# Optimization experiments

Hardware: AMD Instinct MI355X
Metric: run time of the kernel (lower is better)

The kernel has to match this reference:

```python
import jax, jax.numpy as jnp
import numpy as np

# FP4 E2M1 value table (codes 0..7 positive, 8..15 negative, sign in MSB)
FP4_VALUES = jnp.array([0.0, 0.5, 1.0, 1.5, 2.0, 3.0, 4.0, 6.0,
                        -0.0, -0.5, -1.0, -1.5, -2.0, -3.0, -4.0, -6.0],
                       dtype=jnp.float32)


def setup_inputs() -> dict:
    key = jax.random.key(0)
    k1, k2, k3, k4 = jax.random.split(key, 4)
    O, I = 4096, 4096
    block = 16
    x = jax.random.normal(k1, (8192, I), dtype=jnp.float32)
    # packed uint4 pairs stored as int32 bytes in [0, 256)
    weight = jax.random.randint(k2, (O, I // 2), 0, 256, dtype=jnp.int32)
    # per-block FP8-style scales (positive)
    weight_scale = jax.random.uniform(k3, (O, I // block), dtype=jnp.float32, minval=0.01, maxval=1.0)
    bias = jax.random.normal(k4, (O,), dtype=jnp.float32)
    return {"x": x, "weight": weight, "weight_scale": weight_scale,
            "bias": bias, "block_size": block}


def _dequant_nvfp4(weight, weight_scale, block_size):
    # unpack two FP4 codes per byte: high nibble is the even (first) element
    hi = (weight >> 4) & 0xF
    lo = weight & 0xF
    O = weight.shape[0]
    codes = jnp.stack([hi, lo], axis=-1).reshape(O, -1)  # [O, I]
    vals = FP4_VALUES[codes]                             # [O, I] f32
    I = vals.shape[1]
    # apply per-block scale
    w = vals.reshape(O, I // block_size, block_size) * weight_scale[:, :, None]
    return w.reshape(O, I)


def reference(x, weight, weight_scale, bias, block_size):
    w = _dequant_nvfp4(weight, weight_scale, block_size)  # [O, I]
    return jnp.einsum('ti,oi->to', x, w) + bias[None, :]
```

## Files before the change

### kernel.cpp

```cpp
#include <hip/hip_runtime.h>
#include <hip/hip_fp16.h>

typedef __attribute__((ext_vector_type(8))) _Float16 f16x8;
typedef __attribute__((ext_vector_type(4))) float f32x4;

#define M_DIM 8192
#define N_DIM 4096
#define K_DIM 4096
#define BM 256
#define BN 256
#define BK 64
#define NT (K_DIM / BK)
#define ITERS (NT / 2)

__constant__ float FP4_LUT[16] = {0.f, 0.5f, 1.f, 1.5f, 2.f, 3.f, 4.f, 6.f,
                                  -0.f, -0.5f, -1.f, -1.5f, -2.f, -3.f, -4.f, -6.f};

__device__ inline void glds16(const void* g, void* l) {
    __builtin_amdgcn_global_load_lds(
        (const __attribute__((address_space(1))) void*)g,
        (__attribute__((address_space(3))) void*)l, 16, 0, 0);
}

__global__ __launch_bounds__(256) void cvt_x_kernel(const float* __restrict__ x,
                                                    _Float16* __restrict__ xh) {
    int i = (blockIdx.x * 256 + threadIdx.x) * 8;
    const float4* p = (const float4*)(x + i);
    float4 a = p[0], b = p[1];
    f16x8 h;
    h[0] = (_Float16)a.x; h[1] = (_Float16)a.y;
    h[2] = (_Float16)a.z; h[3] = (_Float16)a.w;
    h[4] = (_Float16)b.x; h[5] = (_Float16)b.y;
    h[6] = (_Float16)b.z; h[7] = (_Float16)b.w;
    *(f16x8*)(xh + i) = h;
}

__global__ __launch_bounds__(256) void dequant_w_kernel(const int* __restrict__ w,
                                                        const float* __restrict__ wsc,
                                                        _Float16* __restrict__ wh) {
    int t = blockIdx.x * 256 + threadIdx.x;
    int4 b4 = ((const int4*)w)[t];
    int o  = t >> 9;
    int j0 = (t & 511) << 2;
    float s = wsc[(o << 8) + (j0 >> 3)];
    f16x8 h;
    int b;
    b = b4.x; h[0] = (_Float16)(FP4_LUT[(b >> 4) & 15] * s); h[1] = (_Float16)(FP4_LUT[b & 15] * s);
    b = b4.y; h[2] = (_Float16)(FP4_LUT[(b >> 4) & 15] * s); h[3] = (_Float16)(FP4_LUT[b & 15] * s);
    b = b4.z; h[4] = (_Float16)(FP4_LUT[(b >> 4) & 15] * s); h[5] = (_Float16)(FP4_LUT[b & 15] * s);
    b = b4.w; h[6] = (_Float16)(FP4_LUT[(b >> 4) & 15] * s); h[7] = (_Float16)(FP4_LUT[b & 15] * s);
    *(f16x8*)(wh + ((long)o << 12) + (j0 << 1)) = h;
}


#define VM8 asm volatile("s_waitcnt vmcnt(8)" ::: "memory")
#define VM4 asm volatile("s_waitcnt vmcnt(4)" ::: "memory")
#define VM0 asm volatile("s_waitcnt vmcnt(0)" ::: "memory")
#define VMX ((void)0)

#define STAGE(OP, SD, KH, KOFF) do {                                           \
    _Float16* _d = lds + (SD)*32768 + (OP)*16384 + (KH)*8192 + (wid << 9);     \
    const _Float16* _s = ((OP) ? srcB : srcA) + (KOFF);                        \
    glds16(_s, _d);                                                            \
    glds16(_s + (size_t)128 * K_DIM, _d + 4096);                               \
  } while (0)

#define PHASE(CB, KH, MH, DOB, VMS, ...) do {                                  \
    const _Float16* _cb = lds + (CB)*32768 + (KH)*8192;                        \
    if (DOB) {                                                                 \
      bf[0] = *(const f16x8*)(_cb + b_off);                                    \
      bf[1] = *(const f16x8*)(_cb + b_off + 512);                              \
      bf[2] = *(const f16x8*)(_cb + b_off + 1024);                             \
      bf[3] = *(const f16x8*)(_cb + b_off + 1536);                             \
    }                                                                          \
    af[0] = *(const f16x8*)(_cb + a_off + (MH)*2048);                          \
    af[1] = *(const f16x8*)(_cb + a_off + (MH)*2048 + 512);                    \
    af[2] = *(const f16x8*)(_cb + a_off + (MH)*2048 + 1024);                   \
    af[3] = *(const f16x8*)(_cb + a_off + (MH)*2048 + 1536);                   \
    __VA_ARGS__;                                                               \
    __builtin_amdgcn_s_barrier();                                              \
    asm volatile("s_waitcnt lgkmcnt(0)" ::: "memory");                         \
    __builtin_amdgcn_s_setprio(1);                                             \
    _Pragma("unroll")                                                          \
    for (int mf = 0; mf < 4; ++mf) {                                           \
      _Pragma("unroll")                                                        \
      for (int nf = 0; nf < 4; ++nf)                                           \
        acc[(MH)*4 + mf][nf] = __builtin_amdgcn_mfma_f32_16x16x32_f16(         \
            af[mf], bf[nf], acc[(MH)*4 + mf][nf], 0, 0, 0);                    \
    }                                                                          \
    __builtin_amdgcn_s_setprio(0);                                             \
    VMS;                                                                       \
    __builtin_amdgcn_s_barrier();                                              \
  } while (0)

__global__ __launch_bounds__(512, 2) void gemm_f16_8ph(const _Float16* __restrict__ A,
                                                       const _Float16* __restrict__ B,
                                                       const float* __restrict__ bias,
                                                       float* __restrict__ C) {
    __shared__ _Float16 lds[2 * 32768];

    const int tid  = threadIdx.x;
    const int wid  = tid >> 6;
    const int lane = tid & 63;
    const int fr   = lane & 15;
    const int kg   = lane >> 4;
    const int wm   = wid >> 2;
    const int wn   = wid & 3;

    const int c = blockIdx.x & 7;
    const int q = blockIdx.x >> 3;
    const int bm = (c >> 1) * 8 + (q & 7);
    const int bn = (c & 1) * 8 + (q >> 3);
    const int brow = bm * BM;
    const int bcol = bn * BN;

    const int s_col = (((tid & 3) ^ ((tid >> 3) & 3)) << 3);
    const _Float16* srcA = A + (size_t)(brow + (tid >> 2)) * K_DIM + s_col;
    const _Float16* srcB = B + (size_t)(bcol + (tid >> 2)) * K_DIM + s_col;

    const int swz   = ((kg ^ ((fr >> 1) & 3)) << 3);
    const int a_off = (wm * 128 + fr) * 32 + swz;
    const int b_off = 16384 + (wn * 64 + fr) * 32 + swz;

    f16x8 af[4], bf[4];
    f32x4 acc[8][4] = {};

    STAGE(0, 0, 0, 0);
    STAGE(1, 0, 0, 0);
    STAGE(0, 0, 1, 32);
    STAGE(1, 0, 1, 32);
    STAGE(0, 1, 0, 64);
    STAGE(1, 1, 0, 64);
    VM8;
    __builtin_amdgcn_s_barrier();

    for (int i = 0; i < ITERS - 1; ++i) {
        const int kb = i << 7;
        PHASE(0, 0, 0, true,  VMX, STAGE(0, 1, 1, kb + 96));
        PHASE(0, 0, 1, false, VM8, STAGE(1, 1, 1, kb + 96));
        PHASE(0, 1, 0, true,  VMX, STAGE(0, 0, 0, kb + 128));
        PHASE(0, 1, 1, false, VM8, STAGE(1, 0, 0, kb + 128));
        PHASE(1, 0, 0, true,  VMX, STAGE(0, 0, 1, kb + 160));
        PHASE(1, 0, 1, false, VM8, STAGE(1, 0, 1, kb + 160));
        PHASE(1, 1, 0, true,  VMX, STAGE(0, 1, 0, kb + 192));
        PHASE(1, 1, 1, false, VM8, STAGE(1, 1, 0, kb + 192));
    }
    {
        const int kb = (ITERS - 1) << 7;
        PHASE(0, 0, 0, true,  VMX, STAGE(0, 1, 1, kb + 96));
        PHASE(0, 0, 1, false, VM8, STAGE(1, 1, 1, kb + 96));
        PHASE(0, 1, 0, true,  VMX, VMX);
        PHASE(0, 1, 1, false, VM4, VMX);
        PHASE(1, 0, 0, true,  VMX, VMX);
        PHASE(1, 0, 1, false, VM0, VMX);
        PHASE(1, 1, 0, true,  VMX, VMX);
        PHASE(1, 1, 1, false, VMX, VMX);
    }

#pragma unroll
    for (int m = 0; m < 8; ++m) {
        int row = brow + wm * 128 + m * 16 + kg * 4;
#pragma unroll
        for (int n = 0; n < 4; ++n) {
            int col = bcol + wn * 64 + n * 16 + fr;
            float bv = bias[col];
#pragma unroll
            for (int j = 0; j < 4; ++j)
                __builtin_nontemporal_store(acc[m][n][j] + bv,
                                            &C[(size_t)(row + j) * N_DIM + col]);
        }
    }
}

__global__ __launch_bounds__(256) void fallback_kernel(const float* __restrict__ x,
                                                       const int* __restrict__ w,
                                                       const float* __restrict__ wsc,
                                                       const float* __restrict__ bias,
                                                       float* __restrict__ out) {
    long idx = (long)blockIdx.x * 256 + threadIdx.x;
    int t = (int)(idx >> 12);
    int o = (int)(idx & 4095);
    float acc = 0.f;
    for (int j = 0; j < K_DIM / 2; ++j) {
        int b = w[o * (K_DIM / 2) + j];
        float s = wsc[(o << 8) + (j >> 3)];
        acc += x[(long)t * K_DIM + 2 * j]     * (FP4_LUT[(b >> 4) & 15] * s);
        acc += x[(long)t * K_DIM + 2 * j + 1] * (FP4_LUT[b & 15] * s);
    }
    out[idx] = acc + bias[o];
}

extern "C" void kernel_launch(void* const* d_in, const int* in_sizes, int n_in,
                              void* d_out, int out_size, void* d_ws, size_t ws_size,
                              hipStream_t stream) {
    const float* x    = (const float*)d_in[0];
    const int*   w    = (const int*)d_in[1];
    const float* wsc  = (const float*)d_in[2];
    const float* bias = (const float*)d_in[3];
    float* out = (float*)d_out;

    const size_t xh_bytes = (size_t)M_DIM * K_DIM * 2;
    const size_t wh_bytes = (size_t)N_DIM * K_DIM * 2;

    if (ws_size >= xh_bytes + wh_bytes) {
        _Float16* xh = (_Float16*)d_ws;
        _Float16* wh = (_Float16*)((char*)d_ws + xh_bytes);
        cvt_x_kernel<<<(M_DIM * K_DIM) / (256 * 8), 256, 0, stream>>>(x, xh);
        dequant_w_kernel<<<(N_DIM * (K_DIM / 2)) / (256 * 4), 256, 0, stream>>>(w, wsc, wh);
        gemm_f16_8ph<<<(M_DIM / BM) * (N_DIM / BN), 512, 0, stream>>>(xh, wh, bias, out);
    } else {
        fallback_kernel<<<((long)M_DIM * N_DIM) / 256, 256, 0, stream>>>(x, w, wsc, bias, out);
    }
}
```

Before: 298.8 us.

## Double-buffer MFMA fragments in registers to overlap LDS reads with compute

Restructures the GEMM main loop so the A/B fragments for the next phase are loaded from LDS into a second register set while the current phase's MFMAs run. Each phase now has one barrier instead of two, and it waits on partial lgkmcnt/vmcnt counts rather than draining them fully. Separately, the output epilogue switches from nontemporal stores to plain stores. The extra fragment registers raise VGPR pressure under the 512-thread, 2-block launch bounds, and the hand-tuned wait counts risk reading LDS data that is not yet ready.

```diff
diff --git a/kernel.cpp b/kernel.cpp
--- a/kernel.cpp
+++ b/kernel.cpp
@@ -53,10 +53,14 @@
 }
 
 
-#define VM8 asm volatile("s_waitcnt vmcnt(8)" ::: "memory")
+#define VM6 asm volatile("s_waitcnt vmcnt(6)" ::: "memory")
 #define VM4 asm volatile("s_waitcnt vmcnt(4)" ::: "memory")
+#define VM2 asm volatile("s_waitcnt vmcnt(2)" ::: "memory")
 #define VM0 asm volatile("s_waitcnt vmcnt(0)" ::: "memory")
-#define VMX ((void)0)
+#define LG8 asm volatile("s_waitcnt lgkmcnt(8)" ::: "memory")
+#define LG4 asm volatile("s_waitcnt lgkmcnt(4)" ::: "memory")
+#define LG0 asm volatile("s_waitcnt lgkmcnt(0)" ::: "memory")
+#define NOP ((void)0)
 
 #define STAGE(OP, SD, KH, KOFF) do {                                           \
     _Float16* _d = lds + (SD)*32768 + (OP)*16384 + (KH)*8192 + (wid << 9);     \
@@ -65,38 +69,39 @@
     glds16(_s + (size_t)128 * K_DIM, _d + 4096);                               \
   } while (0)
 
-#define PHASE(CB, KH, MH, DOB, VMS, ...) do {                                  \
-    const _Float16* _cb = lds + (CB)*32768 + (KH)*8192;                        \
-    if (DOB) {                                                                 \
-      bf[0] = *(const f16x8*)(_cb + b_off);                                    \
-      bf[1] = *(const f16x8*)(_cb + b_off + 512);                              \
-      bf[2] = *(const f16x8*)(_cb + b_off + 1024);                             \
-      bf[3] = *(const f16x8*)(_cb + b_off + 1536);                             \
+#define PH(DOAF, NCB, NKH, NMH, AFN, DOBF, BFN, LGW, MHC, AFC, BFC, STG, VMW) do { \
+    STG;                                                                       \
+    const _Float16* _nb = lds + (NCB)*32768 + (NKH)*8192;                      \
+    if (DOAF) {                                                                \
+      AFN[0] = *(const f16x8*)(_nb + a_off + (NMH)*2048);                      \
+      AFN[1] = *(const f16x8*)(_nb + a_off + (NMH)*2048 + 512);                \
+      AFN[2] = *(const f16x8*)(_nb + a_off + (NMH)*2048 + 1024);               \
+      AFN[3] = *(const f16x8*)(_nb + a_off + (NMH)*2048 + 1536);               \
     }                                                                          \
-    af[0] = *(const f16x8*)(_cb + a_off + (MH)*2048);                          \
-    af[1] = *(const f16x8*)(_cb + a_off + (MH)*2048 + 512);                    \
-    af[2] = *(const f16x8*)(_cb + a_off + (MH)*2048 + 1024);                   \
-    af[3] = *(const f16x8*)(_cb + a_off + (MH)*2048 + 1536);                   \
-    __VA_ARGS__;                                                               \
-    __builtin_amdgcn_s_barrier();                                              \
-    asm volatile("s_waitcnt lgkmcnt(0)" ::: "memory");                         \
+    if (DOBF) {                                                                \
+      BFN[0] = *(const f16x8*)(_nb + b_off);                                   \
+      BFN[1] = *(const f16x8*)(_nb + b_off + 512);                             \
+      BFN[2] = *(const f16x8*)(_nb + b_off + 1024);                            \
+      BFN[3] = *(const f16x8*)(_nb + b_off + 1536);                            \
+    }                                                                          \
+    LGW;                                                                       \
     __builtin_amdgcn_s_setprio(1);                                             \
     _Pragma("unroll")                                                          \
     for (int mf = 0; mf < 4; ++mf) {                                           \
       _Pragma("unroll")                                                        \
       for (int nf = 0; nf < 4; ++nf)                                           \
-        acc[(MH)*4 + mf][nf] = __builtin_amdgcn_mfma_f32_16x16x32_f16(         \
-            af[mf], bf[nf], acc[(MH)*4 + mf][nf], 0, 0, 0);                    \
+        acc[(MHC)*4 + mf][nf] = __builtin_amdgcn_mfma_f32_16x16x32_f16(        \
+            AFC[mf], BFC[nf], acc[(MHC)*4 + mf][nf], 0, 0, 0);                 \
     }                                                                          \
     __builtin_amdgcn_s_setprio(0);                                             \
-    VMS;                                                                       \
+    VMW;                                                                       \
     __builtin_amdgcn_s_barrier();                                              \
   } while (0)
 
-__global__ __launch_bounds__(512, 2) void gemm_f16_8ph(const _Float16* __restrict__ A,
-                                                       const _Float16* __restrict__ B,
-                                                       const float* __restrict__ bias,
-                                                       float* __restrict__ C) {
+__global__ __launch_bounds__(512, 2) void gemm_f16_pf(const _Float16* __restrict__ A,
+                                                      const _Float16* __restrict__ B,
+                                                      const float* __restrict__ bias,
+                                                      float* __restrict__ C) {
     __shared__ _Float16 lds[2 * 32768];
 
     const int tid  = threadIdx.x;
@@ -122,7 +127,7 @@
     const int a_off = (wm * 128 + fr) * 32 + swz;
     const int b_off = 16384 + (wn * 64 + fr) * 32 + swz;
 
-    f16x8 af[4], bf[4];
+    f16x8 af0[4], af1[4], bf0[4], bf1[4];
     f32x4 acc[8][4] = {};
 
     STAGE(0, 0, 0, 0);
@@ -131,30 +136,38 @@
     STAGE(1, 0, 1, 32);
     STAGE(0, 1, 0, 64);
     STAGE(1, 1, 0, 64);
-    VM8;
+    VM2;
     __builtin_amdgcn_s_barrier();
+    af0[0] = *(const f16x8*)(lds + a_off);
+    af0[1] = *(const f16x8*)(lds + a_off + 512);
+    af0[2] = *(const f16x8*)(lds + a_off + 1024);
+    af0[3] = *(const f16x8*)(lds + a_off + 1536);
+    bf0[0] = *(const f16x8*)(lds + b_off);
+    bf0[1] = *(const f16x8*)(lds + b_off + 512);
+    bf0[2] = *(const f16x8*)(lds + b_off + 1024);
+    bf0[3] = *(const f16x8*)(lds + b_off + 1536);
 
     for (int i = 0; i < ITERS - 1; ++i) {
         const int kb = i << 7;
-        PHASE(0, 0, 0, true,  VMX, STAGE(0, 1, 1, kb + 96));
-        PHASE(0, 0, 1, false, VM8, STAGE(1, 1, 1, kb + 96));
-        PHASE(0, 1, 0, true,  VMX, STAGE(0, 0, 0, kb + 128));
-        PHASE(0, 1, 1, false, VM8, STAGE(1, 0, 0, kb + 128));
-        PHASE(1, 0, 0, true,  VMX, STAGE(0, 0, 1, kb + 160));
-        PHASE(1, 0, 1, false, VM8, STAGE(1, 0, 1, kb + 160));
-        PHASE(1, 1, 0, true,  VMX, STAGE(0, 1, 0, kb + 192));
-        PHASE(1, 1, 1, false, VM8, STAGE(1, 1, 0, kb + 192));
+        PH(1, 0,0,1, af1, 0,bf0, LG4, 0, af0, bf0, STAGE(0,1,1,kb+96),  VM6);
+        PH(1, 0,1,0, af0, 1,bf1, LG8, 1, af1, bf0, STAGE(1,1,1,kb+96),  NOP);
+        PH(1, 0,1,1, af1, 0,bf0, LG4, 0, af0, bf1, STAGE(0,0,0,kb+128), VM6);
+        PH(1, 1,0,0, af0, 1,bf0, LG8, 1, af1, bf1, STAGE(1,0,0,kb+128), NOP);
+        PH(1, 1,0,1, af1, 0,bf0, LG4, 0, af0, bf0, STAGE(0,0,1,kb+160), VM6);
+        PH(1, 1,1,0, af0, 1,bf1, LG8, 1, af1, bf0, STAGE(1,0,1,kb+160), NOP);
+        PH(1, 1,1,1, af1, 0,bf0, LG4, 0, af0, bf1, STAGE(0,1,0,kb+192), VM6);
+        PH(1, 0,0,0, af0, 1,bf0, LG8, 1, af1, bf1, STAGE(1,1,0,kb+192), NOP);
     }
     {
         const int kb = (ITERS - 1) << 7;
-        PHASE(0, 0, 0, true,  VMX, STAGE(0, 1, 1, kb + 96));
-        PHASE(0, 0, 1, false, VM8, STAGE(1, 1, 1, kb + 96));
-        PHASE(0, 1, 0, true,  VMX, VMX);
-        PHASE(0, 1, 1, false, VM4, VMX);
-        PHASE(1, 0, 0, true,  VMX, VMX);
-        PHASE(1, 0, 1, false, VM0, VMX);
-        PHASE(1, 1, 0, true,  VMX, VMX);
-        PHASE(1, 1, 1, false, VMX, VMX);
+        PH(1, 0,0,1, af1, 0,bf0, LG4, 0, af0, bf0, STAGE(0,1,1,kb+96), VM6);
+        PH(1, 0,1,0, af0, 1,bf1, LG8, 1, af1, bf0, STAGE(1,1,1,kb+96), NOP);
+        PH(1, 0,1,1, af1, 0,bf0, LG4, 0, af0, bf1, NOP,                VM4);
+        PH(1, 1,0,0, af0, 1,bf0, LG8, 1, af1, bf1, NOP,                NOP);
+        PH(1, 1,0,1, af1, 0,bf0, LG4, 0, af0, bf0, NOP,                VM0);
+        PH(1, 1,1,0, af0, 1,bf1, LG8, 1, af1, bf0, NOP,                NOP);
+        PH(1, 1,1,1, af1, 0,bf0, LG4, 0, af0, bf1, NOP,                NOP);
+        PH(0, 0,0,0, af0, 0,bf0, LG0, 1, af1, bf1, NOP,                NOP);
     }
 
 #pragma unroll
@@ -166,8 +179,7 @@
             float bv = bias[col];
 #pragma unroll
             for (int j = 0; j < 4; ++j)
-                __builtin_nontemporal_store(acc[m][n][j] + bv,
-                                            &C[(size_t)(row + j) * N_DIM + col]);
+                C[(size_t)(row + j) * N_DIM + col] = acc[m][n][j] + bv;
         }
     }
 }
@@ -207,7 +219,7 @@
         _Float16* wh = (_Float16*)((char*)d_ws + xh_bytes);
         cvt_x_kernel<<<(M_DIM * K_DIM) / (256 * 8), 256, 0, stream>>>(x, xh);
         dequant_w_kernel<<<(N_DIM * (K_DIM / 2)) / (256 * 4), 256, 0, stream>>>(w, wsc, wh);
-        gemm_f16_8ph<<<(M_DIM / BM) * (N_DIM / BN), 512, 0, stream>>>(xh, wh, bias, out);
+        gemm_f16_pf<<<(M_DIM / BM) * (N_DIM / BN), 512, 0, stream>>>(xh, wh, bias, out);
     } else {
         fallback_kernel<<<((long)M_DIM * N_DIM) / 256, 256, 0, stream>>>(x, w, wsc, bias, out);
     }
```

After: 283.2 us. 1.05x faster.
